# Kernel optimization log

Hardware: AMD Instinct MI355X
Metric: run time of the kernel (lower is better)

## Reference

```python
import jax, jax.numpy as jnp
import numpy as np

B, T = 128, 64          # batch, episode length
OB, AC, L, H = 32, 8, 128, 256  # ob_dim, ac_dim, latent_dim, mlp hidden
N_SUB = 4               # fixed Dopri5 substeps per interval (replaces adaptive PID controller)


def setup_inputs() -> dict:
    key = jax.random.key(0)
    ks = jax.random.split(key, 12)
    g = lambda k, shape, fan: jax.random.normal(k, shape, jnp.float32) / np.sqrt(fan)
    return {
        "ob": jax.random.normal(ks[0], (B, OB), jnp.float32),
        "acs": jax.random.normal(ks[1], (B, T, AC), jnp.float32),
        # strictly increasing timestamps (cumsum of uniform increments)
        "times": jnp.cumsum(jax.random.uniform(ks[2], (B, T), jnp.float32, 0.02, 0.1), axis=1),
        # ob encoder MLP (OB -> H -> L), relu hidden, identity out
        "We0": g(ks[3], (H, OB), OB), "be0": jnp.zeros((H,), jnp.float32),
        "We1": g(ks[4], (L, H), H), "be1": jnp.zeros((L,), jnp.float32),
        # latent dynamics MLP (L -> H -> H -> L)
        "Wd0": g(ks[5], (H, L), L), "bd0": jnp.zeros((H,), jnp.float32),
        "Wd1": g(ks[6], (H, H), H), "bd1": jnp.zeros((H,), jnp.float32),
        "Wd2": g(ks[7], (L, H), H), "bd2": jnp.zeros((L,), jnp.float32),
        # ob decoder MLP (L -> H -> OB)
        "Wo0": g(ks[8], (H, L), L), "bo0": jnp.zeros((H,), jnp.float32),
        "Wo1": g(ks[9], (OB, H), H), "bo1": jnp.zeros((OB,), jnp.float32),
        # GRU cell (input=AC, hidden=L), equinox layout: gates [r, z, n]
        "Wih": g(ks[10], (3 * L, AC), AC), "Whh": g(ks[11], (3 * L, L), L),
        "bih": jnp.zeros((3 * L,), jnp.float32), "bn": jnp.zeros((L,), jnp.float32),
    }


def reference(ob, acs, times, We0, be0, We1, be1, Wd0, bd0, Wd1, bd1, Wd2, bd2,
              Wo0, bo0, Wo1, bo1, Wih, Whh, bih, bn):
    def f(y):  # dynamics MLP on batched latent (B, L) -> (B, L)
        h1 = jax.nn.relu(y @ Wd0.T + bd0)
        h2 = jax.nn.relu(h1 @ Wd1.T + bd1)
        return h2 @ Wd2.T + bd2

    def gru(x, h):  # equinox GRUCell math, batched
        ir, iz, inn = jnp.split(x @ Wih.T + bih, 3, axis=-1)
        hr, hz, hn = jnp.split(h @ Whh.T, 3, axis=-1)
        r = jax.nn.sigmoid(ir + hr)
        z = jax.nn.sigmoid(iz + hz)
        n = jnp.tanh(inn + r * (hn + bn))
        return (1.0 - z) * n + z * h

    def dopri5_step(y, h):  # one Dopri5 (RK45) step, h: (B, 1) per-sample step size
        k1 = f(y)
        k2 = f(y + h * (0.2 * k1))
        k3 = f(y + h * (3/40 * k1 + 9/40 * k2))
        k4 = f(y + h * (44/45 * k1 - 56/15 * k2 + 32/9 * k3))
        k5 = f(y + h * (19372/6561 * k1 - 25360/2187 * k2 + 64448/6561 * k3 - 212/729 * k4))
        k6 = f(y + h * (9017/3168 * k1 - 355/33 * k2 + 46732/5247 * k3 + 49/176 * k4 - 5103/18656 * k5))
        return y + h * (35/384 * k1 + 500/1113 * k3 + 125/192 * k4 - 2187/6784 * k5 + 11/84 * k6)

    def integrate(y, dt):  # integrate latent ODE from 0 to dt with N_SUB fixed Dopri5 steps
        h = (dt / N_SUB)[:, None]
        return jax.lax.fori_loop(0, N_SUB, lambda i, yy: dopri5_step(yy, h), y)

    # encode first observation, consume first action
    latent0 = jax.nn.relu(ob @ We0.T + be0) @ We1.T + be1  # (B, L)
    latent0 = gru(acs[:, 0], latent0)

    dts = jnp.diff(times, axis=1)  # (B, T-1)

    def step(latent, xs):
        ac, dt = xs
        latent = integrate(latent, dt)
        latent = gru(ac, latent)
        return latent, latent

    xs = (jnp.swapaxes(acs[:, 1:], 0, 1), dts.T)  # time-major for scan
    _, lat_seq = jax.lax.scan(step, latent0, xs)  # (T-1, B, L)

    latents = jnp.concatenate([latent0[None], lat_seq], axis=0)  # (T, B, L)
    latents = jnp.swapaxes(latents, 0, 1)  # (B, T, L)

    h1 = jax.nn.relu(latents @ Wo0.T + bo0)
    return h1 @ Wo1.T + bo1  # (B, T, OB)
```

## Files before the change

### kernel.cpp

```cpp
#include <hip/hip_runtime.h>
#include <stdint.h>

#define NBATCH 128
#define NT     64
#define OBD    32
#define ACD    8
#define LDIM   128
#define HDIM   256

typedef _Float16 h2 __attribute__((ext_vector_type(2)));
typedef float    f4 __attribute__((ext_vector_type(4)));

#if defined(__has_builtin)
#  if __has_builtin(__builtin_amdgcn_fdot2)
#    define HAVE_FDOT2 1
#  endif
#endif

__device__ __forceinline__ float dot2f(h2 a, h2 b, float c) {
#ifdef HAVE_FDOT2
  return __builtin_amdgcn_fdot2(a, b, c, false);
#else
  return c + (float)a[0] * (float)b[0] + (float)a[1] * (float)b[1];
#endif
}

__device__ __forceinline__ h2 pkh(float a, float b) {
  h2 r; r[0] = (_Float16)a; r[1] = (_Float16)b; return r;
}

__device__ __forceinline__ h2 bch(float x) { return __builtin_bit_cast(h2, x); }

__device__ __forceinline__ float sigmf(float x) { return 1.0f / (1.0f + expf(-x)); }

#define DOT4(W, I, Q) \
    a0 = dot2f(W[4*(I)+0], bch(Q.x), a0); \
    a1 = dot2f(W[4*(I)+1], bch(Q.y), a1); \
    a2 = dot2f(W[4*(I)+2], bch(Q.z), a2); \
    a3 = dot2f(W[4*(I)+3], bch(Q.w), a3);

__global__ __launch_bounds__(512)
void ode_rnn_kernel(const float* __restrict__ ob,   const float* __restrict__ acs,
                    const float* __restrict__ times,
                    const float* __restrict__ We0,  const float* __restrict__ be0,
                    const float* __restrict__ We1,  const float* __restrict__ be1,
                    const float* __restrict__ Wd0,  const float* __restrict__ bd0,
                    const float* __restrict__ Wd1,  const float* __restrict__ bd1,
                    const float* __restrict__ Wd2,  const float* __restrict__ bd2,
                    const float* __restrict__ Wo0,  const float* __restrict__ bo0,
                    const float* __restrict__ Wo1,  const float* __restrict__ bo1,
                    const float* __restrict__ Wih,  const float* __restrict__ Whh,
                    const float* __restrict__ bih,  const float* __restrict__ bn,
                    float* __restrict__ out)
{
  const int t    = threadIdx.x;
  const int b    = blockIdx.x;
  const int o2   = t & (HDIM - 1);
  const int half = t >> 8;
  const int r    = t & (LDIM - 1);
  const int quad = t >> 7;

  __shared__ __align__(16) float s_lat[LDIM];
  __shared__ __align__(16) float s_k[6][LDIM];
  __shared__ __align__(16) float s_red[HDIM];
  __shared__ __align__(16) float s_r3[3 * LDIM];
  __shared__ __align__(16) float s_dred[512];
  __shared__ __align__(16) float s_tmp[HDIM];
  __shared__ __align__(16) float s_gz[LDIM];
  __shared__ __align__(16) float s_gin[LDIM];
  __shared__ __align__(16) float s_ghn[LDIM];
  __shared__ __align__(16) float s_obs[OBD];
  __shared__ __align__(16) float s_ac[ACD];
  __shared__ __align__(16) h2    s_in16[LDIM / 2];
  __shared__ __align__(16) h2    s_a16[HDIM / 2];
  __shared__ __align__(16) h2    s_b16[HDIM / 2];

  h2 w0[32], w1[64], w2[32], q0[32], q1[8];
  {
    const float2* p = (const float2*)(Wd0 + o2 * LDIM + half * 64);
#pragma unroll
    for (int i = 0; i < 32; ++i) { float2 v = p[i]; w0[i] = pkh(v.x, v.y); }
  }
  {
    const float2* p = (const float2*)(Wd1 + o2 * HDIM + half * 128);
#pragma unroll
    for (int i = 0; i < 64; ++i) { float2 v = p[i]; w1[i] = pkh(v.x, v.y); }
  }
  {
    const float2* p = (const float2*)(Wd2 + r * HDIM + quad * 64);
#pragma unroll
    for (int i = 0; i < 32; ++i) { float2 v = p[i]; w2[i] = pkh(v.x, v.y); }
  }
  {
    const float2* p = (const float2*)(Wo0 + o2 * LDIM + half * 64);
#pragma unroll
    for (int i = 0; i < 32; ++i) { float2 v = p[i]; q0[i] = pkh(v.x, v.y); }
  }
  {
    const float2* p = (const float2*)(Wo1 + (t & 31) * HDIM + (t >> 5) * 16);
#pragma unroll
    for (int i = 0; i < 8; ++i) { float2 v = p[i]; q1[i] = pkh(v.x, v.y); }
  }

  const float bb0  = bd0[o2];
  const float bb1  = bd1[o2];
  const float bb2  = bd2[r];
  const float rb0  = bo0[o2];
  const float rb1  = (t < OBD) ? bo1[t] : 0.0f;
  const float gbA  = (t < 3 * LDIM) ? bih[t] : 0.0f;
  const float bnr  = (t < LDIM) ? bn[t] : 0.0f;
  const float be1r = (t < LDIM) ? be1[t] : 0.0f;

  auto feval = [&](int s) {
    float a0, a1, a2, a3;
    a0 = a1 = a2 = a3 = 0.0f;
    {
      const f4* src = ((const f4*)s_in16) + half * 8;
#pragma unroll
      for (int i = 0; i < 8; ++i) { f4 q = src[i]; DOT4(w0, i, q) }
    }
    if (half) s_red[o2] = a0 + a1 + a2 + a3;
    __syncthreads();
    if (!half) {
      float v = fmaxf(a0 + a1 + a2 + a3 + s_red[o2] + bb0, 0.0f);
      float ov = __shfl_xor(v, 1);
      if (!(t & 1)) s_a16[o2 >> 1] = pkh(v, ov);
    }
    __syncthreads();
    a0 = a1 = a2 = a3 = 0.0f;
    {
      const f4* src = ((const f4*)s_a16) + half * 16;
#pragma unroll
      for (int i = 0; i < 16; ++i) { f4 q = src[i]; DOT4(w1, i, q) }
    }
    if (half) s_red[o2] = a0 + a1 + a2 + a3;
    __syncthreads();
    if (!half) {
      float v = fmaxf(a0 + a1 + a2 + a3 + s_red[o2] + bb1, 0.0f);
      float ov = __shfl_xor(v, 1);
      if (!(t & 1)) s_b16[o2 >> 1] = pkh(v, ov);
    }
    __syncthreads();
    a0 = a1 = a2 = a3 = 0.0f;
    {
      const f4* src = ((const f4*)s_b16) + quad * 8;
#pragma unroll
      for (int i = 0; i < 8; ++i) { f4 q = src[i]; DOT4(w2, i, q) }
    }
    float p = a0 + a1 + a2 + a3;
    if (quad) s_r3[(quad - 1) * LDIM + r] = p;
    __syncthreads();
    if (!quad) s_k[s][r] = p + s_r3[r] + s_r3[LDIM + r] + s_r3[2 * LDIM + r] + bb2;
  };

  auto substep = [&](float hs) {
#pragma unroll 1
    for (int s = 0; s < 6; ++s) {
      if (t < LDIM) {
        float z = s_lat[t];
        if      (s == 1) z += hs * (0.2f * s_k[0][t]);
        else if (s == 2) z += hs * ((3.0f/40.0f)*s_k[0][t] + (9.0f/40.0f)*s_k[1][t]);
        else if (s == 3) z += hs * ((44.0f/45.0f)*s_k[0][t] - (56.0f/15.0f)*s_k[1][t]
                                  + (32.0f/9.0f)*s_k[2][t]);
        else if (s == 4) z += hs * ((19372.0f/6561.0f)*s_k[0][t] - (25360.0f/2187.0f)*s_k[1][t]
                                  + (64448.0f/6561.0f)*s_k[2][t] - (212.0f/729.0f)*s_k[3][t]);
        else if (s == 5) z += hs * ((9017.0f/3168.0f)*s_k[0][t] - (355.0f/33.0f)*s_k[1][t]
                                  + (46732.0f/5247.0f)*s_k[2][t] + (49.0f/176.0f)*s_k[3][t]
                                  - (5103.0f/18656.0f)*s_k[4][t]);
        float ov = __shfl_xor(z, 1);
        if (!(t & 1)) s_in16[t >> 1] = pkh(z, ov);
      }
      __syncthreads();
      feval(s);
    }
    if (t < LDIM) {
      float y = s_lat[t];
      y += hs * ((35.0f/384.0f)*s_k[0][t] + (500.0f/1113.0f)*s_k[2][t]
               + (125.0f/192.0f)*s_k[3][t] - (2187.0f/6784.0f)*s_k[4][t]
               + (11.0f/84.0f)*s_k[5][t]);
      s_lat[t] = y;
    }
  };

  auto gru = [&](int ts) {
    if (t < ACD) s_ac[t] = acs[((size_t)b * NT + ts) * ACD + t];
    __syncthreads();
    float ig = gbA, hg = 0.0f;
    if (t < 3 * LDIM) {
      const float* wi = Wih + t * ACD;
#pragma unroll
      for (int j = 0; j < ACD; ++j) ig += wi[j] * s_ac[j];
      const f4* wh = (const f4*)(Whh + t * LDIM);
      const f4* xl = (const f4*)s_lat;
#pragma unroll
      for (int k2 = 0; k2 < LDIM / 4; ++k2) {
        f4 w = wh[k2], x = xl[k2];
        hg += w.x*x.x + w.y*x.y + w.z*x.z + w.w*x.w;
      }
    }
    if (t >= LDIM && t < 2 * LDIM)       s_gz[t - LDIM] = ig + hg;
    else if (t >= 2 * LDIM && t < 3 * LDIM) { s_gin[t - 2*LDIM] = ig; s_ghn[t - 2*LDIM] = hg; }
    __syncthreads();
    if (t < LDIM) {
      float rg = sigmf(ig + hg);
      float zg = sigmf(s_gz[t]);
      float ng = tanhf(s_gin[t] + rg * (s_ghn[t] + bnr));
      s_lat[t] = (1.0f - zg) * ng + zg * s_lat[t];
    }
    __syncthreads();
  };

  auto decode = [&](int ts) {
    if (t < LDIM / 2) s_in16[t] = pkh(s_lat[2 * t], s_lat[2 * t + 1]);
    __syncthreads();
    float a0 = 0, a1 = 0, a2 = 0, a3 = 0;
    {
      const f4* src = ((const f4*)s_in16) + half * 8;
#pragma unroll
      for (int i = 0; i < 8; ++i) { f4 q = src[i]; DOT4(q0, i, q) }
    }
    if (half) s_red[o2] = a0 + a1 + a2 + a3;
    __syncthreads();
    if (!half) {
      float v = fmaxf(a0 + a1 + a2 + a3 + s_red[o2] + rb0, 0.0f);
      float ov = __shfl_xor(v, 1);
      if (!(t & 1)) s_a16[o2 >> 1] = pkh(v, ov);
    }
    __syncthreads();
    {
      const int sl = t >> 5;
      const f4* src = ((const f4*)s_a16) + sl * 2;
      float b0 = 0, b1 = 0;
#pragma unroll
      for (int i = 0; i < 2; ++i) {
        f4 q = src[i];
        b0 = dot2f(q1[4*i+0], bch(q.x), b0);
        b1 = dot2f(q1[4*i+1], bch(q.y), b1);
        b0 = dot2f(q1[4*i+2], bch(q.z), b0);
        b1 = dot2f(q1[4*i+3], bch(q.w), b1);
      }
      s_dred[t] = b0 + b1;
    }
    __syncthreads();
    if (t < OBD) {
      float s = rb1;
#pragma unroll
      for (int j = 0; j < 16; ++j) s += s_dred[j * OBD + t];
      out[((size_t)b * NT + ts) * OBD + t] = s;
    }
    __syncthreads();
  };

  if (t < OBD) s_obs[t] = ob[b * OBD + t];
  __syncthreads();
  if (t < HDIM) {
    float acc = be0[t];
    const float* wr = We0 + t * OBD;
#pragma unroll
    for (int j = 0; j < OBD; ++j) acc += wr[j] * s_obs[j];
    s_tmp[t] = fmaxf(acc, 0.0f);
  }
  __syncthreads();
  {
    float acc = 0.0f;
    const f4* wr = (const f4*)(We1 + r * HDIM + quad * 64);
    const f4* xs = (const f4*)(s_tmp + quad * 64);
#pragma unroll
    for (int k = 0; k < 16; ++k) {
      f4 w = wr[k], x = xs[k];
      acc += w.x*x.x + w.y*x.y + w.z*x.z + w.w*x.w;
    }
    if (quad) s_r3[(quad - 1) * LDIM + r] = acc;
    __syncthreads();
    if (!quad) s_lat[r] = acc + s_r3[r] + s_r3[LDIM + r] + s_r3[2 * LDIM + r] + be1r;
    __syncthreads();
  }

  gru(0);
  decode(0);

#pragma unroll 1
  for (int ts = 1; ts < NT; ++ts) {
    float dt = times[b * NT + ts] - times[b * NT + ts - 1];
    float hs = 0.25f * dt;
#pragma unroll 1
    for (int sub = 0; sub < 4; ++sub) substep(hs);
    gru(ts);
    decode(ts);
  }
}

extern "C" void kernel_launch(void* const* d_in, const int* in_sizes, int n_in,
                              void* d_out, int out_size, void* d_ws, size_t ws_size,
                              hipStream_t stream) {
  (void)in_sizes; (void)n_in; (void)d_ws; (void)ws_size; (void)out_size;
  const float* ob    = (const float*)d_in[0];
  const float* acs   = (const float*)d_in[1];
  const float* times = (const float*)d_in[2];
  const float* We0   = (const float*)d_in[3];
  const float* be0   = (const float*)d_in[4];
  const float* We1   = (const float*)d_in[5];
  const float* be1   = (const float*)d_in[6];
  const float* Wd0   = (const float*)d_in[7];
  const float* bd0   = (const float*)d_in[8];
  const float* Wd1   = (const float*)d_in[9];
  const float* bd1   = (const float*)d_in[10];
  const float* Wd2   = (const float*)d_in[11];
  const float* bd2   = (const float*)d_in[12];
  const float* Wo0   = (const float*)d_in[13];
  const float* bo0   = (const float*)d_in[14];
  const float* Wo1   = (const float*)d_in[15];
  const float* bo1   = (const float*)d_in[16];
  const float* Wih   = (const float*)d_in[17];
  const float* Whh   = (const float*)d_in[18];
  const float* bih   = (const float*)d_in[19];
  const float* bn    = (const float*)d_in[20];

  ode_rnn_kernel<<<dim3(NBATCH), dim3(512), 0, stream>>>(
      ob, acs, times, We0, be0, We1, be1, Wd0, bd0, Wd1, bd1, Wd2, bd2,
      Wo0, bo0, Wo1, bo1, Wih, Whh, bih, bn, (float*)d_out);
}
```

Baseline: 2.748 ms.

## Interleave split-K partials across adjacent lanes and reduce with shuffles

Remaps the thread-to-output assignment so the split-K partial sums for each output neuron sit in adjacent lanes of one wavefront. They are then combined with xor shuffles instead of shared-memory scratch plus an extra barrier per layer. This removes about one __syncthreads per MLP layer in every Dopri5 stage and in the decoder. It also drops a barrier in the GRU and decode handoff by having the GRU and final substep write the fp16 packed latent directly. Times and actions are preloaded to shared memory, Wih rows are held in registers, and launch_bounds gains a min-blocks hint of 2, which may raise register pressure and cause spills given the large per-thread weight arrays.

```diff
diff --git a/kernel.cpp b/kernel.cpp
--- a/kernel.cpp
+++ b/kernel.cpp
@@ -39,7 +39,7 @@
     a2 = dot2f(W[4*(I)+2], bch(Q.z), a2); \
     a3 = dot2f(W[4*(I)+3], bch(Q.w), a3);
 
-__global__ __launch_bounds__(512)
+__global__ __launch_bounds__(512, 2)
 void ode_rnn_kernel(const float* __restrict__ ob,   const float* __restrict__ acs,
                     const float* __restrict__ times,
                     const float* __restrict__ We0,  const float* __restrict__ be0,
@@ -55,108 +55,114 @@
 {
   const int t    = threadIdx.x;
   const int b    = blockIdx.x;
-  const int o2   = t & (HDIM - 1);
-  const int half = t >> 8;
-  const int r    = t & (LDIM - 1);
-  const int quad = t >> 7;
+  const int p    = t >> 1;
+  const int sub  = t & 1;
+  const int r3   = t >> 2;
+  const int ksub = t & 3;
 
   __shared__ __align__(16) float s_lat[LDIM];
   __shared__ __align__(16) float s_k[6][LDIM];
-  __shared__ __align__(16) float s_red[HDIM];
-  __shared__ __align__(16) float s_r3[3 * LDIM];
-  __shared__ __align__(16) float s_dred[512];
-  __shared__ __align__(16) float s_tmp[HDIM];
   __shared__ __align__(16) float s_gz[LDIM];
   __shared__ __align__(16) float s_gin[LDIM];
   __shared__ __align__(16) float s_ghn[LDIM];
+  __shared__ __align__(16) float s_tmp[HDIM];
   __shared__ __align__(16) float s_obs[OBD];
-  __shared__ __align__(16) float s_ac[ACD];
+  __shared__ __align__(16) float s_times[NT];
+  __shared__ __align__(16) float s_acs[NT * ACD];
   __shared__ __align__(16) h2    s_in16[LDIM / 2];
   __shared__ __align__(16) h2    s_a16[HDIM / 2];
   __shared__ __align__(16) h2    s_b16[HDIM / 2];
 
   h2 w0[32], w1[64], w2[32], q0[32], q1[8];
   {
-    const float2* p = (const float2*)(Wd0 + o2 * LDIM + half * 64);
-#pragma unroll
-    for (int i = 0; i < 32; ++i) { float2 v = p[i]; w0[i] = pkh(v.x, v.y); }
-  }
-  {
-    const float2* p = (const float2*)(Wd1 + o2 * HDIM + half * 128);
-#pragma unroll
-    for (int i = 0; i < 64; ++i) { float2 v = p[i]; w1[i] = pkh(v.x, v.y); }
-  }
-  {
-    const float2* p = (const float2*)(Wd2 + r * HDIM + quad * 64);
-#pragma unroll
-    for (int i = 0; i < 32; ++i) { float2 v = p[i]; w2[i] = pkh(v.x, v.y); }
-  }
-  {
-    const float2* p = (const float2*)(Wo0 + o2 * LDIM + half * 64);
-#pragma unroll
-    for (int i = 0; i < 32; ++i) { float2 v = p[i]; q0[i] = pkh(v.x, v.y); }
-  }
-  {
-    const float2* p = (const float2*)(Wo1 + (t & 31) * HDIM + (t >> 5) * 16);
-#pragma unroll
-    for (int i = 0; i < 8; ++i) { float2 v = p[i]; q1[i] = pkh(v.x, v.y); }
-  }
-
-  const float bb0  = bd0[o2];
-  const float bb1  = bd1[o2];
-  const float bb2  = bd2[r];
-  const float rb0  = bo0[o2];
-  const float rb1  = (t < OBD) ? bo1[t] : 0.0f;
-  const float gbA  = (t < 3 * LDIM) ? bih[t] : 0.0f;
-  const float bnr  = (t < LDIM) ? bn[t] : 0.0f;
-  const float be1r = (t < LDIM) ? be1[t] : 0.0f;
+    const float2* pp = (const float2*)(Wd0 + p * LDIM + sub * 64);
+#pragma unroll
+    for (int i = 0; i < 32; ++i) { float2 v = pp[i]; w0[i] = pkh(v.x, v.y); }
+  }
+  {
+    const float2* pp = (const float2*)(Wd1 + p * HDIM + sub * 128);
+#pragma unroll
+    for (int i = 0; i < 64; ++i) { float2 v = pp[i]; w1[i] = pkh(v.x, v.y); }
+  }
+  {
+    const float2* pp = (const float2*)(Wd2 + r3 * HDIM + ksub * 64);
+#pragma unroll
+    for (int i = 0; i < 32; ++i) { float2 v = pp[i]; w2[i] = pkh(v.x, v.y); }
+  }
+  {
+    const float2* pp = (const float2*)(Wo0 + p * LDIM + sub * 64);
+#pragma unroll
+    for (int i = 0; i < 32; ++i) { float2 v = pp[i]; q0[i] = pkh(v.x, v.y); }
+  }
+  {
+    const float2* pp = (const float2*)(Wo1 + (t >> 4) * HDIM + (t & 15) * 16);
+#pragma unroll
+    for (int i = 0; i < 8; ++i) { float2 v = pp[i]; q1[i] = pkh(v.x, v.y); }
+  }
+  float wi[8];
+  if (t < 3 * LDIM) {
+#pragma unroll
+    for (int j = 0; j < ACD; ++j) wi[j] = Wih[t * ACD + j];
+  } else {
+#pragma unroll
+    for (int j = 0; j < ACD; ++j) wi[j] = 0.0f;
+  }
+
+  const float bb0 = bd0[p];
+  const float bb1 = bd1[p];
+  const float bb2 = bd2[r3];
+  const float rb0 = bo0[p];
+  const float rb1 = bo1[t >> 4];
+  const float gbA = (t < 3 * LDIM) ? bih[t] : 0.0f;
+  const float bnr = (t < LDIM) ? bn[t] : 0.0f;
 
   auto feval = [&](int s) {
-    float a0, a1, a2, a3;
+    float a0, a1, a2, a3, v;
     a0 = a1 = a2 = a3 = 0.0f;
     {
-      const f4* src = ((const f4*)s_in16) + half * 8;
+      const f4* src = ((const f4*)s_in16) + sub * 8;
 #pragma unroll
       for (int i = 0; i < 8; ++i) { f4 q = src[i]; DOT4(w0, i, q) }
     }
-    if (half) s_red[o2] = a0 + a1 + a2 + a3;
-    __syncthreads();
-    if (!half) {
-      float v = fmaxf(a0 + a1 + a2 + a3 + s_red[o2] + bb0, 0.0f);
-      float ov = __shfl_xor(v, 1);
-      if (!(t & 1)) s_a16[o2 >> 1] = pkh(v, ov);
+    v = a0 + a1 + a2 + a3;
+    v += __shfl_xor(v, 1);
+    v = fmaxf(v + bb0, 0.0f);
+    {
+      float ov = __shfl_xor(v, 2);
+      if ((t & 3) == 0) s_a16[t >> 2] = pkh(v, ov);
     }
     __syncthreads();
     a0 = a1 = a2 = a3 = 0.0f;
     {
-      const f4* src = ((const f4*)s_a16) + half * 16;
+      const f4* src = ((const f4*)s_a16) + sub * 16;
 #pragma unroll
       for (int i = 0; i < 16; ++i) { f4 q = src[i]; DOT4(w1, i, q) }
     }
-    if (half) s_red[o2] = a0 + a1 + a2 + a3;
-    __syncthreads();
-    if (!half) {
-      float v = fmaxf(a0 + a1 + a2 + a3 + s_red[o2] + bb1, 0.0f);
-      float ov = __shfl_xor(v, 1);
-      if (!(t & 1)) s_b16[o2 >> 1] = pkh(v, ov);
+    v = a0 + a1 + a2 + a3;
+    v += __shfl_xor(v, 1);
+    v = fmaxf(v + bb1, 0.0f);
+    {
+      float ov = __shfl_xor(v, 2);
+      if ((t & 3) == 0) s_b16[t >> 2] = pkh(v, ov);
     }
     __syncthreads();
     a0 = a1 = a2 = a3 = 0.0f;
     {
-      const f4* src = ((const f4*)s_b16) + quad * 8;
+      const f4* src = ((const f4*)s_b16) + ksub * 8;
 #pragma unroll
       for (int i = 0; i < 8; ++i) { f4 q = src[i]; DOT4(w2, i, q) }
     }
-    float p = a0 + a1 + a2 + a3;
-    if (quad) s_r3[(quad - 1) * LDIM + r] = p;
-    __syncthreads();
-    if (!quad) s_k[s][r] = p + s_r3[r] + s_r3[LDIM + r] + s_r3[2 * LDIM + r] + bb2;
+    v = a0 + a1 + a2 + a3;
+    v += __shfl_xor(v, 1);
+    v += __shfl_xor(v, 2);
+    if ((t & 3) == 0) s_k[s][r3] = v + bb2;
+    __syncthreads();
   };
 
   auto substep = [&](float hs) {
 #pragma unroll 1
     for (int s = 0; s < 6; ++s) {
-      if (t < LDIM) {
+      if (s && t < LDIM) {
         float z = s_lat[t];
         if      (s == 1) z += hs * (0.2f * s_k[0][t]);
         else if (s == 2) z += hs * ((3.0f/40.0f)*s_k[0][t] + (9.0f/40.0f)*s_k[1][t]);
@@ -164,7 +170,7 @@
                                   + (32.0f/9.0f)*s_k[2][t]);
         else if (s == 4) z += hs * ((19372.0f/6561.0f)*s_k[0][t] - (25360.0f/2187.0f)*s_k[1][t]
                                   + (64448.0f/6561.0f)*s_k[2][t] - (212.0f/729.0f)*s_k[3][t]);
-        else if (s == 5) z += hs * ((9017.0f/3168.0f)*s_k[0][t] - (355.0f/33.0f)*s_k[1][t]
+        else             z += hs * ((9017.0f/3168.0f)*s_k[0][t] - (355.0f/33.0f)*s_k[1][t]
                                   + (46732.0f/5247.0f)*s_k[2][t] + (49.0f/176.0f)*s_k[3][t]
                                   - (5103.0f/18656.0f)*s_k[4][t]);
         float ov = __shfl_xor(z, 1);
@@ -179,17 +185,18 @@
                + (125.0f/192.0f)*s_k[3][t] - (2187.0f/6784.0f)*s_k[4][t]
                + (11.0f/84.0f)*s_k[5][t]);
       s_lat[t] = y;
+      float ov = __shfl_xor(y, 1);
+      if (!(t & 1)) s_in16[t >> 1] = pkh(y, ov);
     }
   };
 
   auto gru = [&](int ts) {
-    if (t < ACD) s_ac[t] = acs[((size_t)b * NT + ts) * ACD + t];
     __syncthreads();
     float ig = gbA, hg = 0.0f;
     if (t < 3 * LDIM) {
-      const float* wi = Wih + t * ACD;
-#pragma unroll
-      for (int j = 0; j < ACD; ++j) ig += wi[j] * s_ac[j];
+      const float* xa = s_acs + ts * ACD;
+#pragma unroll
+      for (int j = 0; j < ACD; ++j) ig += wi[j] * xa[j];
       const f4* wh = (const f4*)(Whh + t * LDIM);
       const f4* xl = (const f4*)s_lat;
 #pragma unroll
@@ -198,60 +205,59 @@
         hg += w.x*x.x + w.y*x.y + w.z*x.z + w.w*x.w;
       }
     }
-    if (t >= LDIM && t < 2 * LDIM)       s_gz[t - LDIM] = ig + hg;
+    if (t >= LDIM && t < 2 * LDIM)          s_gz[t - LDIM] = ig + hg;
     else if (t >= 2 * LDIM && t < 3 * LDIM) { s_gin[t - 2*LDIM] = ig; s_ghn[t - 2*LDIM] = hg; }
     __syncthreads();
     if (t < LDIM) {
       float rg = sigmf(ig + hg);
       float zg = sigmf(s_gz[t]);
       float ng = tanhf(s_gin[t] + rg * (s_ghn[t] + bnr));
-      s_lat[t] = (1.0f - zg) * ng + zg * s_lat[t];
-    }
-    __syncthreads();
+      float y  = (1.0f - zg) * ng + zg * s_lat[t];
+      s_lat[t] = y;
+      float ov = __shfl_xor(y, 1);
+      if (!(t & 1)) s_in16[t >> 1] = pkh(y, ov);
+    }
   };
 
   auto decode = [&](int ts) {
-    if (t < LDIM / 2) s_in16[t] = pkh(s_lat[2 * t], s_lat[2 * t + 1]);
-    __syncthreads();
-    float a0 = 0, a1 = 0, a2 = 0, a3 = 0;
-    {
-      const f4* src = ((const f4*)s_in16) + half * 8;
+    __syncthreads();
+    float a0 = 0, a1 = 0, a2 = 0, a3 = 0, v;
+    {
+      const f4* src = ((const f4*)s_in16) + sub * 8;
 #pragma unroll
       for (int i = 0; i < 8; ++i) { f4 q = src[i]; DOT4(q0, i, q) }
     }
-    if (half) s_red[o2] = a0 + a1 + a2 + a3;
-    __syncthreads();
-    if (!half) {
-      float v = fmaxf(a0 + a1 + a2 + a3 + s_red[o2] + rb0, 0.0f);
-      float ov = __shfl_xor(v, 1);
-      if (!(t & 1)) s_a16[o2 >> 1] = pkh(v, ov);
-    }
-    __syncthreads();
-    {
-      const int sl = t >> 5;
-      const f4* src = ((const f4*)s_a16) + sl * 2;
-      float b0 = 0, b1 = 0;
+    v = a0 + a1 + a2 + a3;
+    v += __shfl_xor(v, 1);
+    v = fmaxf(v + rb0, 0.0f);
+    {
+      float ov = __shfl_xor(v, 2);
+      if ((t & 3) == 0) s_a16[t >> 2] = pkh(v, ov);
+    }
+    __syncthreads();
+    a0 = a1 = a2 = a3 = 0;
+    {
+      const f4* src = ((const f4*)s_a16) + (t & 15) * 2;
 #pragma unroll
       for (int i = 0; i < 2; ++i) {
         f4 q = src[i];
-        b0 = dot2f(q1[4*i+0], bch(q.x), b0);
-        b1 = dot2f(q1[4*i+1], bch(q.y), b1);
-        b0 = dot2f(q1[4*i+2], bch(q.z), b0);
-        b1 = dot2f(q1[4*i+3], bch(q.w), b1);
+        a0 = dot2f(q1[4*i+0], bch(q.x), a0);
+        a1 = dot2f(q1[4*i+1], bch(q.y), a1);
+        a2 = dot2f(q1[4*i+2], bch(q.z), a2);
+        a3 = dot2f(q1[4*i+3], bch(q.w), a3);
       }
-      s_dred[t] = b0 + b1;
-    }
-    __syncthreads();
-    if (t < OBD) {
-      float s = rb1;
-#pragma unroll
-      for (int j = 0; j < 16; ++j) s += s_dred[j * OBD + t];
-      out[((size_t)b * NT + ts) * OBD + t] = s;
-    }
-    __syncthreads();
+    }
+    v = a0 + a1 + a2 + a3;
+    v += __shfl_xor(v, 1);
+    v += __shfl_xor(v, 2);
+    v += __shfl_xor(v, 4);
+    v += __shfl_xor(v, 8);
+    if ((t & 15) == 0) out[((size_t)b * NT + ts) * OBD + (t >> 4)] = v + rb1;
   };
 
   if (t < OBD) s_obs[t] = ob[b * OBD + t];
+  if (t < NT)  s_times[t] = times[b * NT + t];
+  s_acs[t] = acs[(size_t)b * NT * ACD + t];
   __syncthreads();
   if (t < HDIM) {
     float acc = be0[t];
@@ -262,18 +268,17 @@
   }
   __syncthreads();
   {
+    const f4* wr = (const f4*)(We1 + r3 * HDIM + ksub * 64);
+    const f4* xs = (const f4*)(s_tmp + ksub * 64);
     float acc = 0.0f;
-    const f4* wr = (const f4*)(We1 + r * HDIM + quad * 64);
-    const f4* xs = (const f4*)(s_tmp + quad * 64);
 #pragma unroll
     for (int k = 0; k < 16; ++k) {
       f4 w = wr[k], x = xs[k];
       acc += w.x*x.x + w.y*x.y + w.z*x.z + w.w*x.w;
     }
-    if (quad) s_r3[(quad - 1) * LDIM + r] = acc;
-    __syncthreads();
-    if (!quad) s_lat[r] = acc + s_r3[r] + s_r3[LDIM + r] + s_r3[2 * LDIM + r] + be1r;
-    __syncthreads();
+    acc += __shfl_xor(acc, 1);
+    acc += __shfl_xor(acc, 2);
+    if ((t & 3) == 0) s_lat[r3] = acc + be1[r3];
   }
 
   gru(0);
@@ -281,10 +286,9 @@
 
 #pragma unroll 1
   for (int ts = 1; ts < NT; ++ts) {
-    float dt = times[b * NT + ts] - times[b * NT + ts - 1];
-    float hs = 0.25f * dt;
+    float hs = 0.25f * (s_times[ts] - s_times[ts - 1]);
 #pragma unroll 1
-    for (int sub = 0; sub < 4; ++sub) substep(hs);
+    for (int su = 0; su < 4; ++su) substep(hs);
     gru(ts);
     decode(ts);
   }
```

After: 2.605 ms. 1.05x faster.
